# Optimization experiments

Measured on AMD Instinct MI355X. Metric: run time of the kernel, lower is better.

The kernel has to match this reference:

```python
import jax, jax.numpy as jnp
import numpy as np

NUM_AGENTS = 64
FEAT_DIM = 524288  # per-agent hidden/state width


def setup_inputs() -> dict:
    key = jax.random.key(0)
    k_h, k_c, k_H, k_C = jax.random.split(key, 4)
    h = jax.random.normal(k_h, (NUM_AGENTS, FEAT_DIM), dtype=jnp.float32)
    c = jax.random.normal(k_c, (NUM_AGENTS, FEAT_DIM), dtype=jnp.float32)
    # learned parameters (torch.randn init in the original module)
    H = jax.random.normal(k_H, (NUM_AGENTS, NUM_AGENTS), dtype=jnp.float32)
    C = jax.random.normal(k_C, (NUM_AGENTS, NUM_AGENTS), dtype=jnp.float32)
    return {"h": h, "c": c, "H": H, "C": C}


def reference(h, c, H, C):
    # hidden = tanh(H @ h + C @ c), shapes: [N,N]@[N,D] -> [N,D]
    hidden = jnp.tanh(jnp.matmul(H, h) + jnp.matmul(C, c))
    # Faithful to source: order[i] stacks hidden[i] (N-1) times and divides
    # by (N-1), so comm[i] == hidden[i] exactly.
    comm = hidden
    return (hidden, comm)
```

## Files before the change

### kernel.cpp

```cpp
#include <hip/hip_runtime.h>

#define NA 64
#define FD 524288
#define FD2 (FD / 2)
#define ROWS 16

__global__ __launch_bounds__(256) void linlayer_kernel(
    const float* __restrict__ h, const float* __restrict__ c,
    const float* __restrict__ Hm, const float* __restrict__ Cm,
    float* __restrict__ out)
{
    const int lane = threadIdx.x & 63;
    int i0 = (threadIdx.x >> 6) * ROWS;
    i0 = __builtin_amdgcn_readfirstlane(i0);

    const int col2 = blockIdx.x * 64 + lane;

    const float2* __restrict__ h2 = (const float2*)h;
    const float2* __restrict__ c2 = (const float2*)c;
    float2* __restrict__ o2 = (float2*)out;

    const float* __restrict__ Hr = Hm + i0 * NA;
    const float* __restrict__ Cr = Cm + i0 * NA;

    float2 acc[ROWS];
#pragma unroll
    for (int i = 0; i < ROWS; ++i) { acc[i].x = 0.f; acc[i].y = 0.f; }

    float2 hv = h2[col2];
    float2 cv = c2[col2];

#pragma unroll 1
    for (int j = 0; j < NA; ++j) {
        const int jn = (j + 1) & (NA - 1);
        const float2 hn = h2[(size_t)jn * FD2 + col2];
        const float2 cn = c2[(size_t)jn * FD2 + col2];
#pragma unroll
        for (int i = 0; i < ROWS; ++i) {
            const float Hij = Hr[i * NA + j];
            const float Cij = Cr[i * NA + j];
            acc[i].x = fmaf(Hij, hv.x, fmaf(Cij, cv.x, acc[i].x));
            acc[i].y = fmaf(Hij, hv.y, fmaf(Cij, cv.y, acc[i].y));
        }
        hv = hn; cv = cn;
    }

#pragma unroll
    for (int i = 0; i < ROWS; ++i) {
        float2 t;
        { const float e = __expf(2.0f * acc[i].x); t.x = 1.0f - 2.0f / (e + 1.0f); }
        { const float e = __expf(2.0f * acc[i].y); t.y = 1.0f - 2.0f / (e + 1.0f); }
        o2[(size_t)(i0 + i) * FD2 + col2] = t;
        o2[(size_t)(NA + i0 + i) * FD2 + col2] = t;
    }
}

extern "C" void kernel_launch(void* const* d_in, const int* in_sizes, int n_in,
                              void* d_out, int out_size, void* d_ws, size_t ws_size,
                              hipStream_t stream) {
    const float* h  = (const float*)d_in[0];
    const float* c  = (const float*)d_in[1];
    const float* Hm = (const float*)d_in[2];
    const float* Cm = (const float*)d_in[3];
    float* out = (float*)d_out;

    dim3 block(256);
    dim3 grid(FD2 / 64);
    hipLaunchKernelGGL(linlayer_kernel, grid, block, 0, stream,
                       h, c, Hm, Cm, out);
}
```

Baseline: 488.8 us.

## Stage transposed weights in LDS and deepen h/c prefetch to four rows

Each block now loads the 64x64 H and C matrices into shared memory in transposed form, so the coefficients for one input row come in as float4 LDS reads instead of scalar loads per row. The single-step prefetch of h and c becomes a four-deep rotating register buffer, putting more global loads in flight per wave. The costs are an extra 32 KB of LDS and a barrier per block, plus more registers, which may lower occupancy. The transpose writes into LDS may also hit bank conflicts.

```diff
diff --git a/kernel.cpp b/kernel.cpp
--- a/kernel.cpp
+++ b/kernel.cpp
@@ -4,14 +4,29 @@
 #define FD 524288
 #define FD2 (FD / 2)
 #define ROWS 16
+#define PF 4
 
 __global__ __launch_bounds__(256) void linlayer_kernel(
     const float* __restrict__ h, const float* __restrict__ c,
     const float* __restrict__ Hm, const float* __restrict__ Cm,
     float* __restrict__ out)
 {
-    const int lane = threadIdx.x & 63;
-    int i0 = (threadIdx.x >> 6) * ROWS;
+    __shared__ float HT[NA * NA];
+    __shared__ float CT[NA * NA];
+
+    const int t = threadIdx.x;
+
+#pragma unroll
+    for (int k = 0; k < 16; ++k) {
+        const int idx = k * 256 + t;
+        const int i = idx >> 6, j = idx & 63;
+        HT[j * NA + i] = Hm[idx];
+        CT[j * NA + i] = Cm[idx];
+    }
+    __syncthreads();
+
+    const int lane = t & 63;
+    int i0 = (t >> 6) * ROWS;
     i0 = __builtin_amdgcn_readfirstlane(i0);
 
     const int col2 = blockIdx.x * 64 + lane;
@@ -20,38 +35,59 @@
     const float2* __restrict__ c2 = (const float2*)c;
     float2* __restrict__ o2 = (float2*)out;
 
-    const float* __restrict__ Hr = Hm + i0 * NA;
-    const float* __restrict__ Cr = Cm + i0 * NA;
-
     float2 acc[ROWS];
 #pragma unroll
     for (int i = 0; i < ROWS; ++i) { acc[i].x = 0.f; acc[i].y = 0.f; }
 
-    float2 hv = h2[col2];
-    float2 cv = c2[col2];
+    float2 hb[PF], cb[PF];
+#pragma unroll
+    for (int p = 0; p < PF; ++p) {
+        hb[p] = h2[(size_t)p * FD2 + col2];
+        cb[p] = c2[(size_t)p * FD2 + col2];
+    }
+
+    const float4* __restrict__ HT4 = (const float4*)HT;
+    const float4* __restrict__ CT4 = (const float4*)CT;
+    const int q0 = i0 >> 2;
 
 #pragma unroll 1
-    for (int j = 0; j < NA; ++j) {
-        const int jn = (j + 1) & (NA - 1);
-        const float2 hn = h2[(size_t)jn * FD2 + col2];
-        const float2 cn = c2[(size_t)jn * FD2 + col2];
+    for (int jo = 0; jo < NA; jo += PF) {
 #pragma unroll
-        for (int i = 0; i < ROWS; ++i) {
-            const float Hij = Hr[i * NA + j];
-            const float Cij = Cr[i * NA + j];
-            acc[i].x = fmaf(Hij, hv.x, fmaf(Cij, cv.x, acc[i].x));
-            acc[i].y = fmaf(Hij, hv.y, fmaf(Cij, cv.y, acc[i].y));
+        for (int p = 0; p < PF; ++p) {
+            const int j = jo + p;
+
+            float Hc[ROWS], Cc[ROWS];
+#pragma unroll
+            for (int q = 0; q < ROWS / 4; ++q) {
+                const float4 hq = HT4[j * (NA / 4) + q0 + q];
+                const float4 cq = CT4[j * (NA / 4) + q0 + q];
+                Hc[4 * q + 0] = hq.x; Hc[4 * q + 1] = hq.y;
+                Hc[4 * q + 2] = hq.z; Hc[4 * q + 3] = hq.w;
+                Cc[4 * q + 0] = cq.x; Cc[4 * q + 1] = cq.y;
+                Cc[4 * q + 2] = cq.z; Cc[4 * q + 3] = cq.w;
+            }
+
+            const float2 hv = hb[p], cv = cb[p];
+
+            const int jn = (j + PF) & (NA - 1);
+            hb[p] = h2[(size_t)jn * FD2 + col2];
+            cb[p] = c2[(size_t)jn * FD2 + col2];
+
+#pragma unroll
+            for (int i = 0; i < ROWS; ++i) {
+                acc[i].x = fmaf(Hc[i], hv.x, fmaf(Cc[i], cv.x, acc[i].x));
+                acc[i].y = fmaf(Hc[i], hv.y, fmaf(Cc[i], cv.y, acc[i].y));
+            }
         }
-        hv = hn; cv = cn;
     }
 
 #pragma unroll
     for (int i = 0; i < ROWS; ++i) {
-        float2 t;
-        { const float e = __expf(2.0f * acc[i].x); t.x = 1.0f - 2.0f / (e + 1.0f); }
-        { const float e = __expf(2.0f * acc[i].y); t.y = 1.0f - 2.0f / (e + 1.0f); }
-        o2[(size_t)(i0 + i) * FD2 + col2] = t;
-        o2[(size_t)(NA + i0 + i) * FD2 + col2] = t;
+        float2 tv;
+        { const float e = __expf(2.0f * acc[i].x); tv.x = 1.0f - 2.0f / (e + 1.0f); }
+        { const float e = __expf(2.0f * acc[i].y); tv.y = 1.0f - 2.0f / (e + 1.0f); }
+        o2[(size_t)(i0 + i) * FD2 + col2] = tv;
+        o2[(size_t)(NA + i0 + i) * FD2 + col2] = tv;
     }
 }
 
```

Result: slower. 526.2 us (+7.7%).

## Pre-transpose coefficient matrices into packed workspace and use 8 rows per wave

Applied to the files above, without the earlier changes.

Adds a small pre-kernel that interleaves the H and C coefficients so that each wave's per-j coefficients sit contiguously in a workspace buffer. The main kernel then fetches them with four float4 loads, prefetched one iteration ahead, instead of 32 scalar loads per j. Each wave now covers 8 output rows, so a block holds 512 threads (8 waves) to still cover all 64 rows. This cuts scalar load traffic and register pressure, which may raise occupancy. The cost is an extra kernel launch and half as much reuse of each h/c load per wave.

```diff
diff --git a/kernel.cpp b/kernel.cpp
--- a/kernel.cpp
+++ b/kernel.cpp
@@ -3,16 +3,30 @@
 #define NA 64
 #define FD 524288
 #define FD2 (FD / 2)
-#define ROWS 16
+#define ROWS 8
 
-__global__ __launch_bounds__(256) void linlayer_kernel(
+__global__ void transpose_coeff(const float* __restrict__ Hm,
+                                const float* __restrict__ Cm,
+                                float* __restrict__ W)
+{
+    const int j = blockIdx.x;
+    const int t = threadIdx.x;
+    const int w = t >> 4;
+    const int k = t & 15;
+    const int row = w * ROWS + (k & 7);
+    const float v = (k < 8) ? Hm[row * NA + j] : Cm[row * NA + j];
+    W[j * 128 + t] = v;
+}
+
+__global__ __launch_bounds__(512) void linlayer_kernel(
     const float* __restrict__ h, const float* __restrict__ c,
-    const float* __restrict__ Hm, const float* __restrict__ Cm,
-    float* __restrict__ out)
+    const float* __restrict__ W, float* __restrict__ out)
 {
-    const int lane = threadIdx.x & 63;
-    int i0 = (threadIdx.x >> 6) * ROWS;
-    i0 = __builtin_amdgcn_readfirstlane(i0);
+    const int t = threadIdx.x;
+    const int lane = t & 63;
+    int wb = (t >> 6) << 4;
+    wb = __builtin_amdgcn_readfirstlane(wb);
+    const int i0 = wb >> 1;
 
     const int col2 = blockIdx.x * 64 + lane;
 
@@ -20,38 +34,42 @@
     const float2* __restrict__ c2 = (const float2*)c;
     float2* __restrict__ o2 = (float2*)out;
 
-    const float* __restrict__ Hr = Hm + i0 * NA;
-    const float* __restrict__ Cr = Cm + i0 * NA;
-
     float2 acc[ROWS];
 #pragma unroll
     for (int i = 0; i < ROWS; ++i) { acc[i].x = 0.f; acc[i].y = 0.f; }
 
+    const float4* __restrict__ W0 = (const float4*)(W + wb);
+    float4 Ha = W0[0], Hb = W0[1], Ca = W0[2], Cb = W0[3];
     float2 hv = h2[col2];
     float2 cv = c2[col2];
 
 #pragma unroll 1
     for (int j = 0; j < NA; ++j) {
         const int jn = (j + 1) & (NA - 1);
+        const float4* __restrict__ Wn = (const float4*)(W + jn * 128 + wb);
+        const float4 Han = Wn[0], Hbn = Wn[1], Can = Wn[2], Cbn = Wn[3];
         const float2 hn = h2[(size_t)jn * FD2 + col2];
         const float2 cn = c2[(size_t)jn * FD2 + col2];
+
+        const float Hc[ROWS] = {Ha.x, Ha.y, Ha.z, Ha.w, Hb.x, Hb.y, Hb.z, Hb.w};
+        const float Cc[ROWS] = {Ca.x, Ca.y, Ca.z, Ca.w, Cb.x, Cb.y, Cb.z, Cb.w};
 #pragma unroll
         for (int i = 0; i < ROWS; ++i) {
-            const float Hij = Hr[i * NA + j];
-            const float Cij = Cr[i * NA + j];
-            acc[i].x = fmaf(Hij, hv.x, fmaf(Cij, cv.x, acc[i].x));
-            acc[i].y = fmaf(Hij, hv.y, fmaf(Cij, cv.y, acc[i].y));
+            acc[i].x = fmaf(Hc[i], hv.x, fmaf(Cc[i], cv.x, acc[i].x));
+            acc[i].y = fmaf(Hc[i], hv.y, fmaf(Cc[i], cv.y, acc[i].y));
         }
+
+        Ha = Han; Hb = Hbn; Ca = Can; Cb = Cbn;
         hv = hn; cv = cn;
     }
 
 #pragma unroll
     for (int i = 0; i < ROWS; ++i) {
-        float2 t;
-        { const float e = __expf(2.0f * acc[i].x); t.x = 1.0f - 2.0f / (e + 1.0f); }
-        { const float e = __expf(2.0f * acc[i].y); t.y = 1.0f - 2.0f / (e + 1.0f); }
-        o2[(size_t)(i0 + i) * FD2 + col2] = t;
-        o2[(size_t)(NA + i0 + i) * FD2 + col2] = t;
+        float2 tv;
+        { const float e = __expf(2.0f * acc[i].x); tv.x = 1.0f - 2.0f / (e + 1.0f); }
+        { const float e = __expf(2.0f * acc[i].y); tv.y = 1.0f - 2.0f / (e + 1.0f); }
+        o2[(size_t)(i0 + i) * FD2 + col2] = tv;
+        o2[(size_t)(NA + i0 + i) * FD2 + col2] = tv;
     }
 }
 
@@ -63,9 +81,12 @@
     const float* Hm = (const float*)d_in[2];
     const float* Cm = (const float*)d_in[3];
     float* out = (float*)d_out;
+    float* W   = (float*)d_ws;
 
-    dim3 block(256);
+    hipLaunchKernelGGL(transpose_coeff, dim3(NA), dim3(128), 0, stream,
+                       Hm, Cm, W);
+    dim3 block(512);
     dim3 grid(FD2 / 64);
     hipLaunchKernelGGL(linlayer_kernel, grid, block, 0, stream,
-                       h, c, Hm, Cm, out);
+                       h, c, W, out);
 }
```

New measurement: 562.8 us. +15.1%, slower.
